# Kernel tuning notes

Hardware: AMD Instinct MI355X
Metric: run time of the kernel (lower is better)

The kernel has to match this reference:

```python
import jax, jax.numpy as jnp
import numpy as np

BLOCK = 64      # base classifier input height/width
STRIDE = 16     # BLOCK // 4 per Windowing(stride=[1,bh/4,bw/4,1], size=[1,bh,bw,1])
K = 10          # n_classes
THRESH = 0.7    # bbox_threshold


def extract_patches(x):
    # x: [B,H,W,C] -> [B,R,Cc,BLOCK*BLOCK*C], same layout as tf.image.extract_patches
    B, H, Wd, C = x.shape
    R = (H - BLOCK) // STRIDE + 1
    Cc = (Wd - BLOCK) // STRIDE + 1
    rows = jnp.arange(R)[:, None] * STRIDE + jnp.arange(BLOCK)[None, :]   # [R,64]
    cols = jnp.arange(Cc)[:, None] * STRIDE + jnp.arange(BLOCK)[None, :]  # [Cc,64]
    p = x[:, rows]                 # [B,R,64,W,C]
    p = p[:, :, :, cols]           # [B,R,64,Cc,64,C]
    p = jnp.transpose(p, (0, 1, 3, 2, 4, 5))  # [B,R,Cc,64,64,C]
    return p.reshape(B, R, Cc, BLOCK * BLOCK * C)


def connected_components(mask):
    # 4-connected components of a 2D bool mask via iterative min-label propagation.
    # Background = 0; foreground labels are distinct positive ints per component.
    R, C = mask.shape
    big = jnp.int32(R * C + 2)
    init = jnp.where(mask, jnp.arange(1, R * C + 1, dtype=jnp.int32).reshape(R, C), 0)

    def step(lab, _):
        l = jnp.where(mask, lab, big)
        up = jnp.concatenate([jnp.full((1, C), big, l.dtype), l[:-1]], 0)
        dn = jnp.concatenate([l[1:], jnp.full((1, C), big, l.dtype)], 0)
        lf = jnp.concatenate([jnp.full((R, 1), big, l.dtype), l[:, :-1]], 1)
        rt = jnp.concatenate([l[:, 1:], jnp.full((R, 1), big, l.dtype)], 1)
        m = jnp.minimum(jnp.minimum(l, jnp.minimum(up, dn)), jnp.minimum(lf, rt))
        return jnp.where(mask, m, 0), None

    lab, _ = jax.lax.scan(step, init, None, length=2 * (R + C))
    return lab


def boxes_from_labels(lab):
    # Segmented min/max over label ids replaces the per-region python loop:
    # box = [rowmin-1, colmin-1, rowmax+1, colmax+1] per component.
    R, C = lab.shape
    N = R * C
    flat = lab.reshape(N)
    rr = jnp.arange(N, dtype=jnp.int32) // C
    cc = jnp.arange(N, dtype=jnp.int32) % C
    rmin = jax.ops.segment_min(rr, flat, num_segments=N + 1)
    cmin = jax.ops.segment_min(cc, flat, num_segments=N + 1)
    rmax = jax.ops.segment_max(rr, flat, num_segments=N + 1)
    cmax = jax.ops.segment_max(cc, flat, num_segments=N + 1)
    cnt = jax.ops.segment_sum(jnp.ones(N, jnp.int32), flat, num_segments=N + 1)
    valid = (cnt > 0).at[0].set(False)  # slot 0 is background
    boxes = jnp.stack([rmin - 1, cmin - 1, rmax + 1, cmax + 1], -1)
    boxes = jnp.where(valid[:, None], boxes, 0)
    return boxes, valid


def setup_inputs() -> dict:
    key = jax.random.key(0)
    k1, k2, k3 = jax.random.split(key, 3)
    inputs = jax.random.normal(k1, (1, 1024, 1024, 3), dtype=jnp.float32)
    # scale W so logits have ~unit variance -> sparse (realistic) threshold mask
    W = jax.random.normal(k2, (12288, K), dtype=jnp.float32) * 0.01
    b = jax.random.normal(k3, (K,), dtype=jnp.float32)
    return {"inputs": inputs, "W": W, "b": b}


def reference(inputs, W, b):
    patches = extract_patches(inputs)               # [1,R,Cc,D]
    B, R, Cc, D = patches.shape
    logits = patches.reshape(B * R * Cc, D) @ W + b # [N,K]
    prob = jax.nn.softmax(logits, axis=1).reshape(R, Cc, K)
    mask = prob > THRESH                            # [R,Cc,K]
    labels = jax.vmap(connected_components, in_axes=2, out_axes=2)(mask)  # [R,Cc,K]
    boxes, valid = jax.vmap(boxes_from_labels)(jnp.transpose(labels, (2, 0, 1)))
    # boxes: [K, R*Cc+1, 4] padded per-component bboxes; valid: [K, R*Cc+1]
    return prob, labels, boxes, valid
```

## Files before the change

### kernel.cpp

```cpp
#include <hip/hip_runtime.h>
#include <cmath>

#define KCLS 10
#define NCELL 3721
#define BIGV  0x0FFFFFFF

#define OUT_PROB 0
#define OUT_LAB  37210
#define OUT_BOX  74420
#define OUT_VALID 223300

#define DPPADD(x, ctrl) \
    x += __int_as_float(__builtin_amdgcn_update_dpp( \
        0, __float_as_int(x), ctrl, 0xf, 0xf, true))

__device__ __forceinline__ float wave_sum64(float x) {
    DPPADD(x, 0x111);
    DPPADD(x, 0x112);
    DPPADD(x, 0x114);
    DPPADD(x, 0x118);
    DPPADD(x, 0x142);
    DPPADD(x, 0x143);
    return x;
}

__global__ __launch_bounds__(256) void k0_transpose(
    const float* __restrict__ W, float* __restrict__ WT)
{
    const int d = blockIdx.x * 256 + threadIdx.x;
    const float2 a0 = *(const float2*)(W + (size_t)d * KCLS + 0);
    const float2 a1 = *(const float2*)(W + (size_t)d * KCLS + 2);
    const float2 a2 = *(const float2*)(W + (size_t)d * KCLS + 4);
    const float2 a3 = *(const float2*)(W + (size_t)d * KCLS + 6);
    const float2 a4 = *(const float2*)(W + (size_t)d * KCLS + 8);
    WT[0 * 12288 + d] = a0.x;  WT[1 * 12288 + d] = a0.y;
    WT[2 * 12288 + d] = a1.x;  WT[3 * 12288 + d] = a1.y;
    WT[4 * 12288 + d] = a2.x;  WT[5 * 12288 + d] = a2.y;
    WT[6 * 12288 + d] = a3.x;  WT[7 * 12288 + d] = a3.y;
    WT[8 * 12288 + d] = a4.x;  WT[9 * 12288 + d] = a4.y;
}

__global__ __launch_bounds__(512, 4) void k1a_logits(
    const float* __restrict__ x, const float* __restrict__ WT,
    const float* __restrict__ b, float* __restrict__ out)
{
    const int tid = threadIdx.x;
    const int r   = blockIdx.x >> 3;
    const int cg  = blockIdx.x & 7;
    const int c0  = (cg == 7) ? 53 : cg * 8;
    __shared__ float red[8][8][KCLS];

    float acc[8][KCLS];
#pragma unroll
    for (int p = 0; p < 8; ++p)
#pragma unroll
        for (int k = 0; k < KCLS; ++k) acc[p][k] = 0.0f;

    int i = (2 * tid) / 192;
    int t = (2 * tid) - i * 192;
    const float* wtb = WT + 2 * tid;

    for (int u = 0; u < 12; ++u) {
        const float* xb = x + (size_t)(r * 16 + i) * 3072 + 48 * c0 + t;
        const float* wb = wtb + (u << 10);

        float2 wt[KCLS];
#pragma unroll
        for (int k = 0; k < KCLS; ++k) wt[k] = *(const float2*)(wb + 12288 * k);

        float2 xv[4];
#pragma unroll
        for (int p = 0; p < 4; ++p) xv[p] = *(const float2*)(xb + 48 * p);
#pragma unroll
        for (int p = 0; p < 4; ++p)
#pragma unroll
            for (int k = 0; k < KCLS; ++k)
                acc[p][k] += xv[p].x * wt[k].x + xv[p].y * wt[k].y;

#pragma unroll
        for (int p = 0; p < 4; ++p) xv[p] = *(const float2*)(xb + 192 + 48 * p);
#pragma unroll
        for (int p = 0; p < 4; ++p)
#pragma unroll
            for (int k = 0; k < KCLS; ++k)
                acc[4 + p][k] += xv[p].x * wt[k].x + xv[p].y * wt[k].y;

        t += 64; i += 5;
        if (t >= 192) { t -= 192; ++i; }
    }

    const int w = tid >> 6;
#pragma unroll
    for (int p = 0; p < 8; ++p)
#pragma unroll
        for (int k = 0; k < KCLS; ++k) {
            const float s = wave_sum64(acc[p][k]);
            if ((tid & 63) == 63) red[w][p][k] = s;
        }
    __syncthreads();

    if (tid < 8) {
        const int cc = c0 + tid;
        double l[KCLS];
#pragma unroll
        for (int k = 0; k < KCLS; ++k) {
            double s = (double)b[k];
#pragma unroll
            for (int w2 = 0; w2 < 8; ++w2) s += (double)red[w2][tid][k];
            l[k] = s;
        }
        double m = l[0];
#pragma unroll
        for (int k = 1; k < KCLS; ++k) m = fmax(m, l[k]);
        double e[KCLS], ssum = 0.0;
#pragma unroll
        for (int k = 0; k < KCLS; ++k) { e[k] = exp(l[k] - m); ssum += e[k]; }
        const double inv = 1.0 / ssum;
        float* po = out + OUT_PROB + (size_t)(r * 61 + cc) * KCLS;
#pragma unroll
        for (int k = 0; k < KCLS; ++k) po[k] = (float)(e[k] * inv);
    }
}

__global__ __launch_bounds__(1024) void k2_cc_boxes(float* __restrict__ out)
{
    const int k   = blockIdx.x;
    const int tid = threadIdx.x;

    __shared__ int lab[63 * 64];
    __shared__ int act[NCELL];
    __shared__ int nact, changed;
    __shared__ int rmn[NCELL + 1], rmx[NCELL + 1], cmn[NCELL + 1], cmx[NCELL + 1];

    for (int idx = tid; idx < 63 * 64; idx += 1024) lab[idx] = BIGV;
    for (int s = tid; s <= NCELL; s += 1024) {
        rmn[s] = 0x7fffffff; cmn[s] = 0x7fffffff; rmx[s] = -1; cmx[s] = -1;
    }
    if (tid == 0) nact = 0;
    __syncthreads();

    for (int idx = tid; idx < NCELL; idx += 1024) {
        const float pv = out[OUT_PROB + (size_t)idx * KCLS + k];
        if (pv > 0.7f) {
            const int r = idx / 61, c = idx - r * 61;
            const int off = (r + 1) * 64 + (c + 1);
            lab[off] = off;
            act[atomicAdd(&nact, 1)] = off;
        }
    }
    __syncthreads();
    const int na = nact;

    for (int round = 0; round < 128; ++round) {
        if (tid == 0) changed = 0;
        __syncthreads();
        bool ch = false;
        for (int ii = tid; ii < na; ii += 1024) {
            const int off = act[ii];
            const int v = lab[off];
            int m = v, t;
            t = lab[off - 1];  if (t < m) m = t;
            t = lab[off + 1];  if (t < m) m = t;
            t = lab[off - 64]; if (t < m) m = t;
            t = lab[off + 64]; if (t < m) m = t;
            if (m < v) {
                int p = lab[m];
                while (p < m) { m = p; p = lab[m]; }
                atomicMin(&lab[off], m);
                atomicMin(&lab[v],   m);
                ch = true;
            }
        }
        if (ch) changed = 1;
        __syncthreads();
        if (changed == 0) break;
        __syncthreads();
    }

    for (int idx = tid; idx < NCELL; idx += 1024) {
        const int r = idx / 61, c = idx - r * 61;
        const int v = lab[(r + 1) * 64 + (c + 1)];
        const int lv = (v < BIGV) ? ((v >> 6) * 61 - 61 + (v & 63)) : 0;
        out[OUT_LAB + (size_t)idx * KCLS + k] = (float)lv;
    }

    for (int ii = tid; ii < na; ii += 1024) {
        const int off = act[ii];
        const int v = lab[off];
        const int lb = (v >> 6) * 61 - 61 + (v & 63);
        const int r = (off >> 6) - 1, c = (off & 63) - 1;
        atomicMin(&rmn[lb], r); atomicMax(&rmx[lb], r);
        atomicMin(&cmn[lb], c); atomicMax(&cmx[lb], c);
    }
    __syncthreads();

    for (int s = tid; s <= NCELL; s += 1024) {
        const bool val = (s > 0) && (rmx[s] >= 0);
        float* bo = out + OUT_BOX + (size_t)(k * (NCELL + 1) + s) * 4;
        if (val) {
            bo[0] = (float)(rmn[s] - 1);
            bo[1] = (float)(cmn[s] - 1);
            bo[2] = (float)(rmx[s] + 1);
            bo[3] = (float)(cmx[s] + 1);
        } else {
            bo[0] = 0.0f; bo[1] = 0.0f; bo[2] = 0.0f; bo[3] = 0.0f;
        }
        out[OUT_VALID + (size_t)k * (NCELL + 1) + s] = val ? 1.0f : 0.0f;
    }
}

extern "C" void kernel_launch(void* const* d_in, const int* in_sizes, int n_in,
                              void* d_out, int out_size, void* d_ws, size_t ws_size,
                              hipStream_t stream) {
    const float* x = (const float*)d_in[0];
    const float* W = (const float*)d_in[1];
    const float* b = (const float*)d_in[2];
    float* out = (float*)d_out;
    float* WT  = (float*)d_ws;

    k0_transpose<<<dim3(48),  dim3(256),  0, stream>>>(W, WT);
    k1a_logits  <<<dim3(488), dim3(512),  0, stream>>>(x, WT, b, out);
    k2_cc_boxes <<<dim3(KCLS), dim3(1024), 0, stream>>>(out);
}
```

Measured before the change: 114.7 us.

## Split logits reduction dimension into four partial blocks with separate softmax kernel

The logits kernel now splits the 12288-long dot product into four quarters handled by separate 256-thread blocks, giving 1952 blocks instead of 488. Partial sums go to a workspace buffer, and a new kernel adds them with the bias in double precision and applies the softmax. This is meant to raise parallelism and occupancy (waves_per_eu set to 3) in the memory-bound GEMV-like stage. The cost is an extra kernel launch and a round trip through global memory for the partial sums.

```diff
diff --git a/kernel.cpp b/kernel.cpp
--- a/kernel.cpp
+++ b/kernel.cpp
@@ -40,15 +40,18 @@
     WT[8 * 12288 + d] = a4.x;  WT[9 * 12288 + d] = a4.y;
 }
 
-__global__ __launch_bounds__(512, 4) void k1a_logits(
+__global__ __launch_bounds__(256)
+__attribute__((amdgpu_waves_per_eu(3, 3))) void k1a_partial(
     const float* __restrict__ x, const float* __restrict__ WT,
-    const float* __restrict__ b, float* __restrict__ out)
+    float* __restrict__ partial)
 {
     const int tid = threadIdx.x;
-    const int r   = blockIdx.x >> 3;
-    const int cg  = blockIdx.x & 7;
+    const int bid = blockIdx.x;
+    const int q   = bid & 3;
+    const int cg  = (bid >> 2) & 7;
+    const int r   = bid >> 5;
     const int c0  = (cg == 7) ? 53 : cg * 8;
-    __shared__ float red[8][8][KCLS];
+    __shared__ float red[4][8][KCLS];
 
     float acc[8][KCLS];
 #pragma unroll
@@ -56,13 +59,14 @@
 #pragma unroll
         for (int k = 0; k < KCLS; ++k) acc[p][k] = 0.0f;
 
-    int i = (2 * tid) / 192;
-    int t = (2 * tid) - i * 192;
-    const float* wtb = WT + 2 * tid;
-
-    for (int u = 0; u < 12; ++u) {
+    const int dq = 3072 * q + 2 * tid;
+    int i = dq / 192;
+    int t = dq - i * 192;
+    const float* wtb = WT + dq;
+
+    for (int u = 0; u < 6; ++u) {
         const float* xb = x + (size_t)(r * 16 + i) * 3072 + 48 * c0 + t;
-        const float* wb = wtb + (u << 10);
+        const float* wb = wtb + (u << 9);
 
         float2 wt[KCLS];
 #pragma unroll
@@ -85,7 +89,7 @@
             for (int k = 0; k < KCLS; ++k)
                 acc[4 + p][k] += xv[p].x * wt[k].x + xv[p].y * wt[k].y;
 
-        t += 64; i += 5;
+        t += 128; i += 2;
         if (t >= 192) { t -= 192; ++i; }
     }
 
@@ -99,16 +103,35 @@
         }
     __syncthreads();
 
-    if (tid < 8) {
-        const int cc = c0 + tid;
+    if (tid < 80) {
+        const int p = tid / 10, k = tid - p * 10;
+        const float s = red[0][p][k] + red[1][p][k] + red[2][p][k] + red[3][p][k];
+        partial[(size_t)q * 37210 + (size_t)r * 610 + (size_t)(c0 + p) * 10 + k] = s;
+    }
+}
+
+__global__ __launch_bounds__(640) void k1b_softmax(
+    const float* __restrict__ partial, const float* __restrict__ b,
+    float* __restrict__ out)
+{
+    const int r   = blockIdx.x;
+    const int tid = threadIdx.x;
+    __shared__ double lgs[61][KCLS];
+
+    if (tid < 610) {
+        const int c = tid / 10, k = tid - c * 10;
+        const float* p = partial + (size_t)r * 610 + tid;
+        double s = (double)b[k];
+#pragma unroll
+        for (int q = 0; q < 4; ++q) s += (double)p[(size_t)q * 37210];
+        lgs[c][k] = s;
+    }
+    __syncthreads();
+
+    if (tid < 61) {
         double l[KCLS];
 #pragma unroll
-        for (int k = 0; k < KCLS; ++k) {
-            double s = (double)b[k];
-#pragma unroll
-            for (int w2 = 0; w2 < 8; ++w2) s += (double)red[w2][tid][k];
-            l[k] = s;
-        }
+        for (int k = 0; k < KCLS; ++k) l[k] = lgs[tid][k];
         double m = l[0];
 #pragma unroll
         for (int k = 1; k < KCLS; ++k) m = fmax(m, l[k]);
@@ -116,7 +139,7 @@
 #pragma unroll
         for (int k = 0; k < KCLS; ++k) { e[k] = exp(l[k] - m); ssum += e[k]; }
         const double inv = 1.0 / ssum;
-        float* po = out + OUT_PROB + (size_t)(r * 61 + cc) * KCLS;
+        float* po = out + OUT_PROB + (size_t)(r * 61 + tid) * KCLS;
 #pragma unroll
         for (int k = 0; k < KCLS; ++k) po[k] = (float)(e[k] * inv);
     }
@@ -215,10 +238,12 @@
     const float* x = (const float*)d_in[0];
     const float* W = (const float*)d_in[1];
     const float* b = (const float*)d_in[2];
-    float* out = (float*)d_out;
-    float* WT  = (float*)d_ws;
-
-    k0_transpose<<<dim3(48),  dim3(256),  0, stream>>>(W, WT);
-    k1a_logits  <<<dim3(488), dim3(512),  0, stream>>>(x, WT, b, out);
+    float* out     = (float*)d_out;
+    float* WT      = (float*)d_ws;
+    float* partial = (float*)d_ws + 10 * 12288;
+
+    k0_transpose<<<dim3(48),   dim3(256),  0, stream>>>(W, WT);
+    k1a_partial <<<dim3(1952), dim3(256),  0, stream>>>(x, WT, partial);
+    k1b_softmax <<<dim3(61),   dim3(640),  0, stream>>>(partial, b, out);
     k2_cc_boxes <<<dim3(KCLS), dim3(1024), 0, stream>>>(out);
 }
```

New measurement: 128.1 us. +11.7%, slower.
